# Performance work log

Measured on AMD Instinct MI355X. Metric: run time of the kernel, lower is better.

Reference implementation:

```python
import jax, jax.numpy as jnp
import numpy as np

B, S, W, D, T = 64, 512, 384, 768, 21


def setup_inputs() -> dict:
    key = jax.random.key(0)
    ks = jax.random.split(key, 8)
    hidden_states = jax.random.normal(ks[0], (B, S, D), dtype=jnp.float32)  # BERT last_hidden_state
    word_maps = jnp.sort(jax.random.randint(ks[1], (B, W), 0, S), axis=1)  # first-subword index per word
    tags = jax.random.randint(ks[2], (B, W), 0, T)
    word_mask = jnp.ones((B, W), dtype=bool)  # torchcrf requires mask[:,0] all on
    W_tag = jax.random.normal(ks[3], (T, D), dtype=jnp.float32) * 0.02  # hidden2tag weight
    b_tag = jnp.zeros((T,), dtype=jnp.float32)
    start_trans = jax.random.uniform(ks[4], (T,), minval=-0.1, maxval=0.1)
    end_trans = jax.random.uniform(ks[5], (T,), minval=-0.1, maxval=0.1)
    trans = jax.random.uniform(ks[6], (T, T), minval=-0.1, maxval=0.1)
    return dict(hidden_states=hidden_states, W_tag=W_tag, b_tag=b_tag,
                start_trans=start_trans, end_trans=end_trans, trans=trans,
                word_maps=word_maps, tags=tags, word_mask=word_mask)


def reference(hidden_states, W_tag, b_tag, start_trans, end_trans, trans,
              word_maps, tags, word_mask):
    # --- ragged subword -> word gather (vectorized form of the python loop) ---
    word_feats = jnp.take_along_axis(hidden_states, word_maps[:, :, None], axis=1)  # [B,W,D]
    # dropout is identity in eval / deterministic reference
    emissions = jnp.einsum('bwd,td->bwt', word_feats, W_tag) + b_tag  # [B,W,T]

    maskf = word_mask.astype(emissions.dtype)
    bidx = jnp.arange(tags.shape[0])

    # --- CRF numerator: score of the given tag sequence ---
    emit_sc = jnp.take_along_axis(emissions, tags[:, :, None], axis=2)[..., 0]  # [B,W]
    trans_sc = trans[tags[:, :-1], tags[:, 1:]]                                  # [B,W-1]
    num = start_trans[tags[:, 0]] + emit_sc[:, 0]
    num = num + jnp.sum((trans_sc + emit_sc[:, 1:]) * maskf[:, 1:], axis=1)
    lengths = word_mask.sum(axis=1)
    last_tags = jnp.take_along_axis(tags, (lengths - 1)[:, None], axis=1)[:, 0]
    num = num + end_trans[last_tags]

    # --- CRF denominator: log partition via forward recurrence (scan over time) ---
    def step(score, xm):
        em_t, m_t = xm  # [B,T], [B]
        nxt = jax.nn.logsumexp(score[:, :, None] + trans[None, :, :] + em_t[:, None, :], axis=1)
        return jnp.where(m_t[:, None], nxt, score), None

    score0 = start_trans[None, :] + emissions[:, 0]  # [B,T]
    score, _ = jax.lax.scan(step, score0,
                            (jnp.swapaxes(emissions[:, 1:], 0, 1), word_mask[:, 1:].T))
    log_z = jax.nn.logsumexp(score + end_trans[None, :], axis=1)  # [B]

    llh = num - log_z
    return -jnp.mean(llh)  # reduction='mean', negated
```

## Files before the change

### kernel.cpp

```cpp
#include <hip/hip_runtime.h>
#include <math.h>

#define BB 64
#define SS 512
#define WW 384
#define DD 768
#define TT 21
#define ROWS (BB*WW)
#define EMSTRIDE (WW*TT)
#define NCH 16
#define CLEN 24
#define PSTRIDE 24
#define PMATSZ (TT*PSTRIDE)
#define LN32 3.4657359027997265f

typedef short   bf16x8 __attribute__((ext_vector_type(8)));
typedef float   f32x4  __attribute__((ext_vector_type(4)));
union FragU { bf16x8 v; unsigned u[4]; };

__device__ __forceinline__ unsigned pack_bf16(unsigned lo, unsigned hi) {
    return __builtin_amdgcn_perm(hi, lo, 0x07060302);
}

__global__ __launch_bounds__(256) void emissions_kernel(
    const float* __restrict__ hidden, const int* __restrict__ word_maps,
    const float* __restrict__ W_tag, const float* __restrict__ b_tag,
    float* __restrict__ em, float* __restrict__ out)
{
    __shared__ __align__(16) unsigned short Bs[24 * 2 * 4 * 16 * 8];
    __shared__ __align__(16) float Sred[2][64][8];
    __shared__ int rowoff[32];

    const int tid = threadIdx.x;
    const int rowBase = blockIdx.x * 32;

    if (blockIdx.x == 0 && tid == 0) out[0] = 0.0f;

    if (tid < 32) {
        int row = rowBase + tid;
        int b = row / WW;
        int w = row - b * WW;
        rowoff[tid] = b * SS + word_maps[b * WW + w];
    }

    for (int i = tid; i < TT * (DD / 4); i += 256) {
        int t = i / (DD / 4), q = i - t * (DD / 4);
        int k  = q * 4;
        int ks = k >> 5, quad = (k >> 3) & 3, e = k & 7;
        int nt = t >> 4, l16 = t & 15;
        float4 wv = *(const float4*)&W_tag[t * DD + k];
        int off = ((ks * 2 + nt) * 4 + quad) * 128 + l16 * 8 + e;
        *(unsigned*)&Bs[off]     = pack_bf16(__float_as_uint(wv.x), __float_as_uint(wv.y));
        *(unsigned*)&Bs[off + 2] = pack_bf16(__float_as_uint(wv.z), __float_as_uint(wv.w));
    }
    __syncthreads();

    const int wv_  = tid >> 6;
    const int rt   = wv_ >> 1;
    const int h    = wv_ & 1;
    const int lane = tid & 63;
    const int l16  = lane & 15;
    const int quad = lane >> 4;

    const float* abase = hidden + (size_t)rowoff[rt * 16 + l16] * DD
                                + h * (DD / 2) + quad * 8;
    const unsigned short* bbase = Bs + quad * 128 + l16 * 8 + h * 12 * 1024;

    f32x4 acc0 = {}, acc1 = {};

    float4 A0[4], A1[4];
    #pragma unroll
    for (int p = 0; p < 4; ++p) {
        A0[p] = *(const float4*)(abase + p * 32);
        A1[p] = *(const float4*)(abase + p * 32 + 4);
    }
    bf16x8 b0c = *(const bf16x8*)(bbase);
    bf16x8 b1c = *(const bf16x8*)(bbase + 512);

    #pragma unroll
    for (int ks = 0; ks < 12; ++ks) {
        bf16x8 b0n = b0c, b1n = b1c;
        if (ks < 11) {
            b0n = *(const bf16x8*)(bbase + (ks + 1) * 1024);
            b1n = *(const bf16x8*)(bbase + (ks + 1) * 1024 + 512);
        }
        FragU a;
        a.u[0] = pack_bf16(__float_as_uint(A0[ks & 3].x), __float_as_uint(A0[ks & 3].y));
        a.u[1] = pack_bf16(__float_as_uint(A0[ks & 3].z), __float_as_uint(A0[ks & 3].w));
        a.u[2] = pack_bf16(__float_as_uint(A1[ks & 3].x), __float_as_uint(A1[ks & 3].y));
        a.u[3] = pack_bf16(__float_as_uint(A1[ks & 3].z), __float_as_uint(A1[ks & 3].w));
        if (ks < 8) {
            A0[ks & 3] = *(const float4*)(abase + (ks + 4) * 32);
            A1[ks & 3] = *(const float4*)(abase + (ks + 4) * 32 + 4);
        }
        acc0 = __builtin_amdgcn_mfma_f32_16x16x32_bf16(a.v, b0c, acc0, 0, 0, 0);
        acc1 = __builtin_amdgcn_mfma_f32_16x16x32_bf16(a.v, b1c, acc1, 0, 0, 0);
        b0c = b0n; b1c = b1n;
    }

    if (h == 1) {
        #pragma unroll
        for (int r = 0; r < 4; ++r) {
            Sred[rt][lane][r]     = acc0[r];
            Sred[rt][lane][r + 4] = acc1[r];
        }
    }
    __syncthreads();

    if (h == 0) {
        #pragma unroll
        for (int r = 0; r < 4; ++r) {
            acc0[r] += Sred[rt][lane][r];
            acc1[r] += Sred[rt][lane][r + 4];
        }
        int rbase = rowBase + rt * 16 + quad * 4;
        {
            float bt = b_tag[l16];
            #pragma unroll
            for (int r = 0; r < 4; ++r)
                em[(size_t)(rbase + r) * TT + l16] = acc0[r] + bt;
        }
        if (16 + l16 < TT) {
            float bt = b_tag[16 + l16];
            #pragma unroll
            for (int r = 0; r < 4; ++r)
                em[(size_t)(rbase + r) * TT + 16 + l16] = acc1[r] + bt;
        }
    }
}

__global__ __launch_bounds__(256) void chunk_kernel(
    const float* __restrict__ em, const float* __restrict__ trans,
    float* __restrict__ Pmat)
{
    __shared__ __align__(16) float Pbuf[4][2][PMATSZ];
    __shared__ __align__(16) float gem[4][CLEN * PSTRIDE];

    const int wid  = threadIdx.x >> 6;
    const int lane = threadIdx.x & 63;
    const int id   = blockIdx.x * 4 + wid;
    const int b    = id >> 4;
    const int c    = id & (NCH - 1);
    const int s0   = 1 + c * CLEN;
    const int n    = (c == NCH - 1) ? (WW - s0) : CLEN;

    int i3r = lane / 6;
    const int jg  = lane - i3r * 6;
    const bool active = (i3r < 7) && (jg < 6);
    const int i3 = (i3r < 7) ? i3r : 6;
    const int jbase = (jg < 6 ? jg : 5) * 4;

    float4 etr[CLEN];
    #pragma unroll
    for (int k = 0; k < CLEN; ++k) {
        float4 e = make_float4(0.f, 0.f, 0.f, 0.f);
        if (k < TT) {
            e.x = (jbase + 0 < TT) ? __expf(trans[k * TT + jbase + 0]) * 0.03125f : 0.f;
            e.y = (jbase + 1 < TT) ? __expf(trans[k * TT + jbase + 1]) * 0.03125f : 0.f;
            e.z = (jbase + 2 < TT) ? __expf(trans[k * TT + jbase + 2]) * 0.03125f : 0.f;
            e.w = (jbase + 3 < TT) ? __expf(trans[k * TT + jbase + 3]) * 0.03125f : 0.f;
        }
        etr[k] = e;
    }

    for (int idx = lane; idx < n * PSTRIDE; idx += 64) {
        int tt = idx / PSTRIDE, j = idx - tt * PSTRIDE;
        float g = 1.0f;
        if (j < TT) g = __expf(em[((size_t)b * WW + (s0 + tt)) * TT + j]);
        gem[wid][idx] = g;
    }

    {
        float4 g = *(const float4*)&gem[wid][0 * PSTRIDE + jbase];
        #pragma unroll
        for (int r = 0; r < 3; ++r) {
            int i = i3 * 3 + r;
            float4 e = etr[i];
            float4 v = make_float4(e.x * g.x, e.y * g.y, e.z * g.z, e.w * g.w);
            if (active) *(float4*)&Pbuf[wid][0][i * PSTRIDE + jbase] = v;
        }
    }
    __syncthreads();

    int pp = 0;
    for (int tt = 1; tt < n; ++tt) {
        float acc[3][4];
        #pragma unroll
        for (int r = 0; r < 3; ++r)
            #pragma unroll
            for (int q = 0; q < 4; ++q) acc[r][q] = 0.f;

        const float* Pc = &Pbuf[wid][pp][0];
        #pragma unroll
        for (int kb = 0; kb < 6; ++kb) {
            float4 p0 = *(const float4*)&Pc[(i3 * 3 + 0) * PSTRIDE + kb * 4];
            float4 p1 = *(const float4*)&Pc[(i3 * 3 + 1) * PSTRIDE + kb * 4];
            float4 p2 = *(const float4*)&Pc[(i3 * 3 + 2) * PSTRIDE + kb * 4];
            #pragma unroll
            for (int kk = 0; kk < 4; ++kk) {
                float4 e = etr[kb * 4 + kk];
                float a = (kk == 0) ? p0.x : (kk == 1) ? p0.y : (kk == 2) ? p0.z : p0.w;
                float bv= (kk == 0) ? p1.x : (kk == 1) ? p1.y : (kk == 2) ? p1.z : p1.w;
                float cv= (kk == 0) ? p2.x : (kk == 1) ? p2.y : (kk == 2) ? p2.z : p2.w;
                acc[0][0] = fmaf(a, e.x, acc[0][0]); acc[0][1] = fmaf(a, e.y, acc[0][1]);
                acc[0][2] = fmaf(a, e.z, acc[0][2]); acc[0][3] = fmaf(a, e.w, acc[0][3]);
                acc[1][0] = fmaf(bv, e.x, acc[1][0]); acc[1][1] = fmaf(bv, e.y, acc[1][1]);
                acc[1][2] = fmaf(bv, e.z, acc[1][2]); acc[1][3] = fmaf(bv, e.w, acc[1][3]);
                acc[2][0] = fmaf(cv, e.x, acc[2][0]); acc[2][1] = fmaf(cv, e.y, acc[2][1]);
                acc[2][2] = fmaf(cv, e.z, acc[2][2]); acc[2][3] = fmaf(cv, e.w, acc[2][3]);
            }
        }
        float4 g = *(const float4*)&gem[wid][tt * PSTRIDE + jbase];
        if (active) {
            #pragma unroll
            for (int r = 0; r < 3; ++r) {
                float4 v = make_float4(acc[r][0] * g.x, acc[r][1] * g.y,
                                       acc[r][2] * g.z, acc[r][3] * g.w);
                *(float4*)&Pbuf[wid][1 - pp][(i3 * 3 + r) * PSTRIDE + jbase] = v;
            }
        }
        pp ^= 1;
    }

    float* dst = Pmat + (size_t)id * PMATSZ;
    for (int idx = lane; idx < PMATSZ; idx += 64)
        dst[idx] = Pbuf[wid][pp][idx];
}

__device__ __forceinline__ float lane_bcast(float v, int l) {
    return __uint_as_float(__builtin_amdgcn_readlane(__float_as_uint(v), l));
}

__global__ __launch_bounds__(64) void combine_kernel(
    const float* __restrict__ Pmat, const float* __restrict__ em,
    const int* __restrict__ tags, const float* __restrict__ start_trans,
    const float* __restrict__ end_trans, const float* __restrict__ trans,
    float* __restrict__ out)
{
    const int b = blockIdx.x;
    const int j = threadIdx.x;
    const bool act = (j < TT);
    const int jc = act ? j : (TT - 1);
    const float* emb = em + (size_t)b * EMSTRIDE;

    float s0v = start_trans[jc] + emb[jc];
    float M = act ? s0v : -1e30f;
    #pragma unroll
    for (int o = 32; o > 0; o >>= 1) M = fmaxf(M, __shfl_xor(M, o));
    float sig = act ? __expf(s0v - M) : 0.0f;

    for (int c = 0; c < NCH; ++c) {
        const float* P = Pmat + (size_t)(b * NCH + c) * PMATSZ;
        float col[TT];
        #pragma unroll
        for (int i = 0; i < TT; ++i) col[i] = P[i * PSTRIDE + jc];
        float a0 = 0.f, a1 = 0.f, a2 = 0.f;
        #pragma unroll
        for (int i = 0; i < TT; i += 3) {
            a0 = fmaf(lane_bcast(sig, i    ), col[i    ], a0);
            a1 = fmaf(lane_bcast(sig, i + 1), col[i + 1], a1);
            a2 = fmaf(lane_bcast(sig, i + 2), col[i + 2], a2);
        }
        float v = act ? (a0 + a1 + a2) : 0.0f;
        float m = v;
        #pragma unroll
        for (int o = 32; o > 0; o >>= 1) m = fmaxf(m, __shfl_xor(m, o));
        int nst = (c == NCH - 1) ? (WW - (1 + c * CLEN)) : CLEN;
        M += __logf(m) + (float)nst * LN32;
        sig = v / m;
    }

    float fin = (act && sig > 0.f) ? (M + __logf(sig) + end_trans[jc]) : -1e30f;
    float mm = fin;
    #pragma unroll
    for (int o = 32; o > 0; o >>= 1) mm = fmaxf(mm, __shfl_xor(mm, o));
    float pe = __expf(fin - mm);
    float ssum = pe;
    #pragma unroll
    for (int o = 32; o > 0; o >>= 1) ssum += __shfl_xor(ssum, o);
    float lz = mm + __logf(ssum);

    const int* tb = tags + b * WW;
    float part = 0.f;
    for (int w = j; w < WW; w += 64) {
        int tw = tb[w];
        float e = emb[w * TT + tw];
        float tsc = (w == 0) ? start_trans[tw] : trans[tb[w - 1] * TT + tw];
        part += tsc + e;
    }
    #pragma unroll
    for (int o = 32; o > 0; o >>= 1) part += __shfl_xor(part, o);

    if (j == 0) {
        float num = part + end_trans[tb[WW - 1]];
        atomicAdd(out, -(num - lz) * (1.0f / BB));
    }
}

extern "C" void kernel_launch(void* const* d_in, const int* in_sizes, int n_in,
                              void* d_out, int out_size, void* d_ws, size_t ws_size,
                              hipStream_t stream) {
    const float* hidden      = (const float*)d_in[0];
    const float* W_tag       = (const float*)d_in[1];
    const float* b_tag       = (const float*)d_in[2];
    const float* start_trans = (const float*)d_in[3];
    const float* end_trans   = (const float*)d_in[4];
    const float* trans       = (const float*)d_in[5];
    const int*   word_maps   = (const int*)  d_in[6];
    const int*   tags        = (const int*)  d_in[7];

    float* out  = (float*)d_out;
    float* em   = (float*)d_ws;
    float* Pmat = (float*)d_ws + (size_t)ROWS * TT;

    emissions_kernel<<<ROWS / 32, 256, 0, stream>>>(hidden, word_maps, W_tag, b_tag, em, out);
    chunk_kernel<<<BB * NCH / 4, 256, 0, stream>>>(em, trans, Pmat);
    combine_kernel<<<BB, 64, 0, stream>>>(Pmat, em, tags, start_trans, end_trans, trans, out);
}
```

Before: 206.4 us.

## Fuse CRF chunk and combine kernels into one per-batch block

The chunk-product and combine kernels are merged into a single kernel with one 1024-thread block per batch element and one wave per chunk. Each chunk's transfer matrix stays in shared memory, and wave 0 runs the sequential combine directly from LDS after a block barrier. This removes the global Pmat round-trip and one kernel launch. In exchange, the work now runs on only 64 blocks with heavy LDS use, so fewer CUs are busy while 15 waves sit idle during the combine phase.

After: 316.9 us. 53.6% more time.

```diff
diff --git a/kernel.cpp b/kernel.cpp
--- a/kernel.cpp
+++ b/kernel.cpp
@@ -21,6 +21,9 @@
 __device__ __forceinline__ unsigned pack_bf16(unsigned lo, unsigned hi) {
     return __builtin_amdgcn_perm(hi, lo, 0x07060302);
 }
+__device__ __forceinline__ float lane_bcast(float v, int l) {
+    return __uint_as_float(__builtin_amdgcn_readlane(__float_as_uint(v), l));
+}
 
 __global__ __launch_bounds__(256) void emissions_kernel(
     const float* __restrict__ hidden, const int* __restrict__ word_maps,
@@ -129,18 +132,18 @@
     }
 }
 
-__global__ __launch_bounds__(256) void chunk_kernel(
-    const float* __restrict__ em, const float* __restrict__ trans,
-    float* __restrict__ Pmat)
+__global__ __launch_bounds__(1024) void crf_fused_kernel(
+    const float* __restrict__ em, const int* __restrict__ tags,
+    const float* __restrict__ start_trans, const float* __restrict__ end_trans,
+    const float* __restrict__ trans, float* __restrict__ out)
 {
-    __shared__ __align__(16) float Pbuf[4][2][PMATSZ];
-    __shared__ __align__(16) float gem[4][CLEN * PSTRIDE];
-
+    __shared__ __align__(16) float Pbuf[NCH][2][PMATSZ];
+    __shared__ __align__(16) float gem[NCH][CLEN * PSTRIDE];
+
+    const int b    = blockIdx.x;
     const int wid  = threadIdx.x >> 6;
     const int lane = threadIdx.x & 63;
-    const int id   = blockIdx.x * 4 + wid;
-    const int b    = id >> 4;
-    const int c    = id & (NCH - 1);
+    const int c    = wid;
     const int s0   = 1 + c * CLEN;
     const int n    = (c == NCH - 1) ? (WW - s0) : CLEN;
 
@@ -180,7 +183,6 @@
             if (active) *(float4*)&Pbuf[wid][0][i * PSTRIDE + jbase] = v;
         }
     }
-    __syncthreads();
 
     int pp = 0;
     for (int tt = 1; tt < n; ++tt) {
@@ -222,23 +224,11 @@
         pp ^= 1;
     }
 
-    float* dst = Pmat + (size_t)id * PMATSZ;
-    for (int idx = lane; idx < PMATSZ; idx += 64)
-        dst[idx] = Pbuf[wid][pp][idx];
-}
-
-__device__ __forceinline__ float lane_bcast(float v, int l) {
-    return __uint_as_float(__builtin_amdgcn_readlane(__float_as_uint(v), l));
-}
-
-__global__ __launch_bounds__(64) void combine_kernel(
-    const float* __restrict__ Pmat, const float* __restrict__ em,
-    const int* __restrict__ tags, const float* __restrict__ start_trans,
-    const float* __restrict__ end_trans, const float* __restrict__ trans,
-    float* __restrict__ out)
-{
-    const int b = blockIdx.x;
-    const int j = threadIdx.x;
+    __syncthreads();
+
+    if (wid != 0) return;
+
+    const int j = lane;
     const bool act = (j < TT);
     const int jc = act ? j : (TT - 1);
     const float* emb = em + (size_t)b * EMSTRIDE;
@@ -249,8 +239,9 @@
     for (int o = 32; o > 0; o >>= 1) M = fmaxf(M, __shfl_xor(M, o));
     float sig = act ? __expf(s0v - M) : 0.0f;
 
-    for (int c = 0; c < NCH; ++c) {
-        const float* P = Pmat + (size_t)(b * NCH + c) * PMATSZ;
+    for (int cc = 0; cc < NCH; ++cc) {
+        int nc = (cc == NCH - 1) ? (WW - (1 + cc * CLEN)) : CLEN;
+        const float* P = &Pbuf[cc][(nc - 1) & 1][0];
         float col[TT];
         #pragma unroll
         for (int i = 0; i < TT; ++i) col[i] = P[i * PSTRIDE + jc];
@@ -265,8 +256,7 @@
         float m = v;
         #pragma unroll
         for (int o = 32; o > 0; o >>= 1) m = fmaxf(m, __shfl_xor(m, o));
-        int nst = (c == NCH - 1) ? (WW - (1 + c * CLEN)) : CLEN;
-        M += __logf(m) + (float)nst * LN32;
+        M += __logf(m) + (float)nc * LN32;
         sig = v / m;
     }
 
@@ -309,11 +299,9 @@
     const int*   word_maps   = (const int*)  d_in[6];
     const int*   tags        = (const int*)  d_in[7];
 
-    float* out  = (float*)d_out;
-    float* em   = (float*)d_ws;
-    float* Pmat = (float*)d_ws + (size_t)ROWS * TT;
+    float* out = (float*)d_out;
+    float* em  = (float*)d_ws;
 
     emissions_kernel<<<ROWS / 32, 256, 0, stream>>>(hidden, word_maps, W_tag, b_tag, em, out);
-    chunk_kernel<<<BB * NCH / 4, 256, 0, stream>>>(em, trans, Pmat);
-    combine_kernel<<<BB, 64, 0, stream>>>(Pmat, em, tags, start_trans, end_trans, trans, out);
-}
+    crf_fused_kernel<<<BB, 1024, 0, stream>>>(em, tags, start_trans, end_trans, trans, out);
+}
```
